# Optimization experiments

Measured on AMD Instinct MI355X. Metric: run time of the kernel, lower is better.

Reference implementation:

```python
import jax, jax.numpy as jnp
import numpy as np

B, D, V, T = 256, 1024, 32000, 64  # num_seqs, hidden dim, vocab, history len


def setup_inputs() -> dict:
    key = jax.random.key(0)
    ks = jax.random.split(key, 8)
    hidden = jax.random.normal(ks[0], (B, D), dtype=jnp.float32)
    embedding = jax.random.normal(ks[1], (V, D), dtype=jnp.float32) * (1.0 / np.sqrt(D))
    output_tokens = jax.random.randint(ks[2], (B, T), 0, V, dtype=jnp.int64)
    presence_penalties = jax.random.uniform(ks[3], (B,), dtype=jnp.float32)
    frequency_penalties = jax.random.uniform(ks[4], (B,), dtype=jnp.float32)
    temperatures = jax.random.uniform(ks[5], (B,), dtype=jnp.float32) + 0.5  # > eps
    top_ps = jax.random.uniform(ks[6], (B,), dtype=jnp.float32) * 0.5 + 0.5  # in [0.5, 1.0)
    top_ks = jax.random.randint(ks[7], (B,), 1, V, dtype=jnp.int64)
    return {
        "hidden": hidden,
        "embedding": embedding,
        "output_tokens": output_tokens,
        "presence_penalties": presence_penalties,
        "frequency_penalties": frequency_penalties,
        "temperatures": temperatures,
        "top_ps": top_ps,
        "top_ks": top_ks,
    }


def reference(hidden, embedding, output_tokens, presence_penalties,
              frequency_penalties, temperatures, top_ps, top_ks):
    # 1) logits = pruned hidden states @ embedding^T  -> [B, V]
    logits = jnp.einsum("bd,vd->bv", hidden, embedding)
    b, v = logits.shape

    # 2) presence/frequency penalties via per-row token histogram (np.bincount equiv)
    rows = jnp.broadcast_to(jnp.arange(b)[:, None], output_tokens.shape)
    counts = jnp.zeros((b, v), logits.dtype).at[rows, output_tokens].add(1.0)
    logits = logits - frequency_penalties[:, None] * counts \
                    - presence_penalties[:, None] * (counts > 0).astype(logits.dtype)

    # 3) temperature scaling
    logits = logits / temperatures[:, None]

    # 4) probabilities
    probs = jax.nn.softmax(logits, axis=-1)

    # 5) top-p / top-k: descending sort, cumsum masks, scatter back via inverse perm
    order = jnp.argsort(-probs, axis=-1)                       # descending order
    probs_sort = jnp.take_along_axis(probs, order, axis=-1)
    probs_cum = jnp.cumsum(probs_sort, axis=-1)
    top_p_mask = (probs_cum - probs_sort) > top_ps[:, None]
    top_k_mask = jnp.arange(v)[None, :] >= top_ks[:, None]
    probs_sort = jnp.where(top_p_mask | top_k_mask, 0.0, probs_sort)
    inv = jnp.argsort(order, axis=-1)
    filtered_probs = jnp.take_along_axis(probs_sort, inv, axis=-1)  # original order
    return filtered_probs
```

## Files before the change

### kernel.cpp

```cpp
#include <hip/hip_runtime.h>
#include <math.h>

#define NB 256
#define NV 32000
#define ND 1024
#define NT 64

#define GN 64
#define ASTR 56
#define NKB 64
#define ASLAB (256 * ASTR)
#define NGBLK (NV / GN)
#define INV2048F 4.8828125e-4f

#define NBIN 1024
#define FIX2 4294967296.0
#define PACK1 (1ull << 48)
#define SMASK ((1ull << 48) - 1ull)

typedef _Float16 f16x8 __attribute__((ext_vector_type(8)));
typedef _Float16 f16x4 __attribute__((ext_vector_type(4)));
typedef float f32x16 __attribute__((ext_vector_type(16)));
typedef __attribute__((address_space(3))) void lds_void;
typedef __attribute__((address_space(1))) void glb_void;

struct RowP2 {
  unsigned long long basePack;
  unsigned long long toppZfix;
  unsigned pfx;
  int ktop;
  float invZ;
  unsigned ustar;
  int m;
  int cEq;
};

__device__ __forceinline__ unsigned mono_enc(float f) {
  unsigned u = __float_as_uint(f);
  return (u & 0x80000000u) ? ~u : (u | 0x80000000u);
}
__device__ __forceinline__ float mono_dec(unsigned u) {
  return (u & 0x80000000u) ? __uint_as_float(u & 0x7FFFFFFFu) : __uint_as_float(~u);
}

__global__ __launch_bounds__(256) void convert_A(const float* __restrict__ hidden,
                                                 _Float16* __restrict__ A3) {
  const int kb = blockIdx.x, t = threadIdx.x;
  __shared__ _Float16 slab[ASLAB];
#pragma unroll
  for (int it = 0; it < 4; it++) {
    const int m = it * 64 + (t >> 2);
    const int k4 = (t & 3) * 4;
    float4 a4 = *(const float4*)(hidden + (size_t)m * ND + kb * 16 + k4);
    _Float16* base = slab + m * ASTR;
    float v[4] = {a4.x, a4.y, a4.z, a4.w};
#pragma unroll
    for (int q = 0; q < 4; q++) {
      const _Float16 h = (_Float16)v[q];
      const _Float16 l2 = (_Float16)((v[q] - (float)h) * 2048.0f);
      const int kk = k4 + q;
      base[kk] = h;
      base[16 + 2 * kk] = h;
      base[17 + 2 * kk] = l2;
    }
  }
  __syncthreads();
  const uint4* s = (const uint4*)slab;
  uint4* g = (uint4*)(A3 + (size_t)kb * ASLAB);
#pragma unroll
  for (int i = 0; i < 7; i++) g[i * 256 + t] = s[i * 256 + t];
}

__global__ __launch_bounds__(256, 2) void gemm_f16s(
    const float* __restrict__ Bm, const _Float16* __restrict__ A3,
    const float* __restrict__ temp, unsigned* __restrict__ rowmax,
    float* __restrict__ C) {
  __shared__ _Float16 Als[ASLAB];
  __shared__ _Float16 Bls[GN * ASTR];
  __shared__ float s_invT[256];
  __shared__ unsigned s_pm[256];

  const int t = threadIdx.x;
  const int l = t & 63, w = t >> 6;
  const int n0 = blockIdx.x * GN;
  s_invT[t] = 1.0f / temp[t];
  s_pm[t] = 0u;

  f32x16 accA[2][2] = {};
  f32x16 accB[2][2] = {};

  const int bn = t >> 2, bk4 = (t & 3) * 4;
  const int l31 = l & 31, lh = l >> 5;
  const int ka = lh * 8;
  const int mb = w * 64;

  for (int kb = 0; kb < NKB; kb++) {
    {
      const char* ga = (const char*)A3 + (size_t)kb * (ASLAB * 2) + (w * 7) * 1024 + l * 16;
      char* la = (char*)Als + (w * 7) * 1024;
#pragma unroll
      for (int i = 0; i < 7; i++)
        __builtin_amdgcn_global_load_lds((const glb_void*)(ga + i * 1024),
                                         (lds_void*)(la + i * 1024), 16, 0, 0);
    }
    {
      const float4 bv = *(const float4*)(Bm + (size_t)(n0 + bn) * ND + kb * 16 + bk4);
      const _Float16 h0 = (_Float16)bv.x, h1 = (_Float16)bv.y,
                     h2 = (_Float16)bv.z, h3 = (_Float16)bv.w;
      const _Float16 l0 = (_Float16)((bv.x - (float)h0) * 2048.0f);
      const _Float16 l1 = (_Float16)((bv.y - (float)h1) * 2048.0f);
      const _Float16 l2 = (_Float16)((bv.z - (float)h2) * 2048.0f);
      const _Float16 l3 = (_Float16)((bv.w - (float)h3) * 2048.0f);
      _Float16* prow = Bls + bn * ASTR;
      *(f16x4*)(prow + bk4) = (f16x4){h0, h1, h2, h3};
      *(f16x8*)(prow + 16 + 2 * bk4) = (f16x8){l0, h0, l1, h1, l2, h2, l3, h3};
    }
    __syncthreads();
    {
      const _Float16* Ap = Als + (size_t)(mb + l31) * ASTR + ka;
      const _Float16* Bp = Bls + (size_t)l31 * ASTR + ka;
      f16x8 a0 = *(const f16x8*)(Ap);
      f16x8 a1 = *(const f16x8*)(Ap + 32 * ASTR);
      f16x8 b0 = *(const f16x8*)(Bp);
      f16x8 b1 = *(const f16x8*)(Bp + 32 * ASTR);
      accA[0][0] = __builtin_amdgcn_mfma_f32_32x32x16_f16(a0, b0, accA[0][0], 0, 0, 0);
      accA[0][1] = __builtin_amdgcn_mfma_f32_32x32x16_f16(a0, b1, accA[0][1], 0, 0, 0);
      accA[1][0] = __builtin_amdgcn_mfma_f32_32x32x16_f16(a1, b0, accA[1][0], 0, 0, 0);
      accA[1][1] = __builtin_amdgcn_mfma_f32_32x32x16_f16(a1, b1, accA[1][1], 0, 0, 0);
#pragma unroll
      for (int s = 0; s < 2; s++) {
        const int off = 16 + s * 16;
        f16x8 c0 = *(const f16x8*)(Ap + off);
        f16x8 c1 = *(const f16x8*)(Ap + 32 * ASTR + off);
        f16x8 d0 = *(const f16x8*)(Bp + off);
        f16x8 d1 = *(const f16x8*)(Bp + 32 * ASTR + off);
        accB[0][0] = __builtin_amdgcn_mfma_f32_32x32x16_f16(c0, d0, accB[0][0], 0, 0, 0);
        accB[0][1] = __builtin_amdgcn_mfma_f32_32x32x16_f16(c0, d1, accB[0][1], 0, 0, 0);
        accB[1][0] = __builtin_amdgcn_mfma_f32_32x32x16_f16(c1, d0, accB[1][0], 0, 0, 0);
        accB[1][1] = __builtin_amdgcn_mfma_f32_32x32x16_f16(c1, d1, accB[1][1], 0, 0, 0);
      }
    }
    __syncthreads();
  }

#pragma unroll
  for (int mi = 0; mi < 2; mi++) {
#pragma unroll
    for (int r = 0; r < 16; r++) {
      const int row = mb + mi * 32 + (r & 3) + 8 * (r >> 2) + 4 * lh;
      const float it = s_invT[row];
      float v0 = (accA[mi][0][r] + accB[mi][0][r] * INV2048F) * it;
      float v1 = (accA[mi][1][r] + accB[mi][1][r] * INV2048F) * it;
      C[(size_t)row * NV + n0 + l31] = v0;
      C[(size_t)row * NV + n0 + 32 + l31] = v1;
      float mx = fmaxf(v0, v1);
#pragma unroll
      for (int o = 1; o < 32; o <<= 1) mx = fmaxf(mx, __shfl_xor(mx, o));
      if (l31 == 0) atomicMax(&s_pm[row], mono_enc(mx));
    }
  }
  __syncthreads();
  atomicMax(&rowmax[t], s_pm[t]);
}

__global__ __launch_bounds__(64) void s0_prep(
    const unsigned* __restrict__ rowmax, const int* __restrict__ toks,
    const float* __restrict__ pres, const float* __restrict__ freq,
    const float* __restrict__ temp, float* __restrict__ Mrow,
    float* __restrict__ buf) {
  const int b = blockIdx.x, t = threadIdx.x;
  __shared__ int s_tok[NT];
  s_tok[t] = toks[b * NT + t];
  __syncthreads();
  const int tk = s_tok[t];
  bool first = true; int cnt = 0;
  for (int j = 0; j < NT; j++)
    if (s_tok[j] == tk) { if (j < t) first = false; cnt++; }
  if (first)
    buf[(size_t)b * NV + tk] -= (freq[b] * (float)cnt + pres[b]) / temp[b];
  if (t == 0) Mrow[b] = mono_dec(rowmax[b]);
}

__global__ __launch_bounds__(256) void h_l0(
    float* __restrict__ buf, const float* __restrict__ Mrow,
    unsigned long long* __restrict__ histP) {
  const int b = blockIdx.x >> 3, sl = blockIdx.x & 7, t = threadIdx.x;
  __shared__ unsigned long long h[NBIN];
  for (int i = t; i < NBIN; i += 256) h[i] = 0ull;
  __syncthreads();
  const float M = Mrow[b];
  float* row = buf + (size_t)b * NV;
  const int base = sl * 4096;
#pragma unroll
  for (int it = 0; it < 4; it++) {
    const int idx = base + (it * 256 + t) * 4;
    if (idx < NV) {
      float4 x4 = *(const float4*)(row + idx);
      float4 e4;
      e4.x = expf(x4.x - M); e4.y = expf(x4.y - M);
      e4.z = expf(x4.z - M); e4.w = expf(x4.w - M);
      *(float4*)(row + idx) = e4;
      unsigned k;
      k = __float_as_uint(e4.x); if (k) atomicAdd(&h[k >> 20], PACK1 | (unsigned long long)(e4.x * FIX2));
      k = __float_as_uint(e4.y); if (k) atomicAdd(&h[k >> 20], PACK1 | (unsigned long long)(e4.y * FIX2));
      k = __float_as_uint(e4.z); if (k) atomicAdd(&h[k >> 20], PACK1 | (unsigned long long)(e4.z * FIX2));
      k = __float_as_uint(e4.w); if (k) atomicAdd(&h[k >> 20], PACK1 | (unsigned long long)(e4.w * FIX2));
    }
  }
  __syncthreads();
  unsigned long long* gh = histP + (size_t)b * NBIN;
  for (int i = t; i < NBIN; i += 256)
    if (h[i]) atomicAdd(&gh[i], h[i]);
}

__global__ __launch_bounds__(256) void h_ref(
    const float* __restrict__ buf, const RowP2* __restrict__ params,
    unsigned long long* __restrict__ histP, int matchShift, int binShift) {
  const int b = blockIdx.x >> 3, sl = blockIdx.x & 7, t = threadIdx.x;
  __shared__ unsigned long long h[NBIN];
  for (int i = t; i < NBIN; i += 256) h[i] = 0ull;
  __syncthreads();
  const unsigned pfx = params[b].pfx;
  const float* row = buf + (size_t)b * NV;
  const int base = sl * 4096;
#pragma unroll
  for (int it = 0; it < 4; it++) {
    const int idx = base + (it * 256 + t) * 4;
    if (idx < NV) {
      float4 e4 = *(const float4*)(row + idx);
      unsigned k;
      k = __float_as_uint(e4.x); if (k && (k >> matchShift) == pfx) atomicAdd(&h[(k >> binShift) & 1023u], PACK1 | (unsigned long long)(e4.x * FIX2));
      k = __float_as_uint(e4.y); if (k && (k >> matchShift) == pfx) atomicAdd(&h[(k >> binShift) & 1023u], PACK1 | (unsigned long long)(e4.y * FIX2));
      k = __float_as_uint(e4.z); if (k && (k >> matchShift) == pfx) atomicAdd(&h[(k >> binShift) & 1023u], PACK1 | (unsigned long long)(e4.z * FIX2));
      k = __float_as_uint(e4.w); if (k && (k >> matchShift) == pfx) atomicAdd(&h[(k >> binShift) & 1023u], PACK1 | (unsigned long long)(e4.w * FIX2));
    }
  }
  __syncthreads();
  unsigned long long* gh = histP + (size_t)b * NBIN;
  for (int i = t; i < NBIN; i += 256)
    if (h[i]) atomicAdd(&gh[i], h[i]);
}

__global__ __launch_bounds__(256) void s2_level(
    unsigned long long* __restrict__ histP, const float* __restrict__ topp_a,
    const int* __restrict__ topk_a, RowP2* __restrict__ params, int level) {
  const int b = blockIdx.x, t = threadIdx.x;
  __shared__ unsigned long long suf[NBIN];
  __shared__ unsigned long long sc[256];
  __shared__ int s_bs;
  unsigned long long* hp = histP + (size_t)b * NBIN;
  unsigned long long v[4];
#pragma unroll
  for (int i = 0; i < 4; i++) { v[i] = hp[t * 4 + i]; hp[t * 4 + i] = 0ull; }
  if (t == 0) s_bs = 1023;
  sc[t] = v[0] + v[1] + v[2] + v[3];
  __syncthreads();
  for (int off = 1; off < 256; off <<= 1) {
    unsigned long long add = (t + off < 256) ? sc[t + off] : 0ull;
    __syncthreads();
    sc[t] += add;
    __syncthreads();
  }
  const unsigned long long totalP = sc[0];
  unsigned long long run = (t < 255) ? sc[t + 1] : 0ull;
  suf[t * 4 + 3] = run; run += v[3];
  suf[t * 4 + 2] = run; run += v[2];
  suf[t * 4 + 1] = run; run += v[1];
  suf[t * 4 + 0] = run;
  __syncthreads();

  RowP2 p;
  unsigned long long base, toppZ;
  int ktop_;
  if (level == 0) {
    ktop_ = topk_a[b];
    unsigned long long Zfix = totalP & SMASK;
    if (!Zfix) Zfix = 1ull;
    toppZ = (unsigned long long)((double)topp_a[b] * (double)Zfix);
    base = 0ull;
    p.pfx = 0; p.invZ = (float)(FIX2 / (double)Zfix);
    p.ustar = 0; p.m = 0; p.cEq = 0;
  } else {
    p = params[b];
    base = p.basePack; toppZ = p.toppZfix; ktop_ = p.ktop;
  }

#pragma unroll
  for (int i = 0; i < 4; i++) {
    const int bin = t * 4 + i;
    const unsigned long long sG = base + suf[bin];
    const bool A = ((long long)(sG >> 48) < (long long)ktop_) && ((sG & SMASK) <= toppZ);
    const unsigned long long sPfull = base + ((bin > 0) ? suf[bin - 1] : totalP);
    const bool Ap = ((long long)(sPfull >> 48) < (long long)ktop_) && ((sPfull & SMASK) <= toppZ);
    if (A && !Ap) s_bs = bin;
  }
  __syncthreads();
  if (t == 0) {
    const int bs = s_bs;
    const unsigned long long newBase = base + suf[bs];
    if (level < 2) {
      p.basePack = newBase;
      p.toppZfix = toppZ;
      p.ktop = ktop_;
      p.pfx = (level == 0) ? (unsigned)bs : ((p.pfx << 10) | (unsigned)bs);
      params[b] = p;
    } else {
      const unsigned ustar = (p.pfx << 10) | (unsigned)bs;
      const unsigned long long raw = ((bs > 0) ? suf[bs - 1] : totalP) - suf[bs];
      const int cEq = (int)(raw >> 48);
      const long long Chi = (long long)(newBase >> 48);
      const unsigned long long Shi = newBase & SMASK;
      long long m = cEq;
      const long long lim = (long long)ktop_ - Chi;
      if (lim < m) m = lim;
      const double tf = (double)__uint_as_float(ustar) * FIX2;
      const double rem = (double)(toppZ - Shi);
      const double Rd = floor(rem / tf) + 1.0;
      if (Rd < (double)m) m = (long long)Rd;
      if (m < 1) m = 1;
      p.ustar = ustar; p.m = (int)m; p.cEq = cEq;
      params[b] = p;
    }
  }
}

__global__ __launch_bounds__(256) void s3_filter(
    float* __restrict__ buf, const RowP2* __restrict__ params) {
  const int b = blockIdx.x >> 3, sl = blockIdx.x & 7, t = threadIdx.x;
  const RowP2 p = params[b];
  const unsigned ustar = p.ustar;
  const float invZ = p.invZ;
  const bool need = (p.m < p.cEq);
  float* row = buf + (size_t)b * NV;
  const int base = sl * 4096;
#pragma unroll
  for (int it = 0; it < 4; it++) {
    const int idx = base + (it * 256 + t) * 4;
    if (idx < NV) {
      float4 e4 = *(const float4*)(row + idx);
      float4 o4;
      unsigned k;
      k = __float_as_uint(e4.x);
      o4.x = (k > ustar) ? e4.x * invZ : ((k == ustar) ? (need ? -e4.x : e4.x * invZ) : 0.f);
      k = __float_as_uint(e4.y);
      o4.y = (k > ustar) ? e4.y * invZ : ((k == ustar) ? (need ? -e4.y : e4.y * invZ) : 0.f);
      k = __float_as_uint(e4.z);
      o4.z = (k > ustar) ? e4.z * invZ : ((k == ustar) ? (need ? -e4.z : e4.z * invZ) : 0.f);
      k = __float_as_uint(e4.w);
      o4.w = (k > ustar) ? e4.w * invZ : ((k == ustar) ? (need ? -e4.w : e4.w * invZ) : 0.f);
      *(float4*)(row + idx) = o4;
    }
  }
}

__global__ __launch_bounds__(256) void s5_tie(
    float* __restrict__ buf, const RowP2* __restrict__ params) {
  const int b = blockIdx.x, t = threadIdx.x;
  const RowP2 p = params[b];
  if (p.m >= p.cEq) return;
  const int m = p.m;
  const float invZ = p.invZ;
  float* row = buf + (size_t)b * NV;
  __shared__ int s_rank[256];
  const int CH = NV / 256;
  const int base = t * CH, end = base + CH;
  int myc = 0;
  for (int v = base; v < end; v++) myc += (row[v] < 0.f);
  s_rank[t] = myc;
  __syncthreads();
  for (int off = 1; off < 256; off <<= 1) {
    const int v0 = s_rank[t];
    const int vn = (t >= off) ? s_rank[t - off] : 0;
    __syncthreads();
    s_rank[t] = v0 + vn;
    __syncthreads();
  }
  int r = (t > 0) ? s_rank[t - 1] : 0;
  for (int v = base; v < end; v++) {
    const float f = row[v];
    if (f < 0.f) {
      row[v] = (r < m) ? (-f) * invZ : 0.f;
      r++;
    }
  }
}

extern "C" void kernel_launch(void* const* d_in, const int* in_sizes, int n_in,
                              void* d_out, int out_size, void* d_ws, size_t ws_size,
                              hipStream_t stream) {
  (void)in_sizes; (void)n_in; (void)out_size; (void)ws_size;
  const float* hidden = (const float*)d_in[0];
  const float* emb    = (const float*)d_in[1];
  const int*   toks   = (const int*)d_in[2];
  const float* pres   = (const float*)d_in[3];
  const float* freq   = (const float*)d_in[4];
  const float* temp   = (const float*)d_in[5];
  const float* topp   = (const float*)d_in[6];
  const int*   topk   = (const int*)d_in[7];
  float* out = (float*)d_out;

  const size_t offA3   = 0;
  const size_t offRM   = 1835008;
  const size_t offHist = offRM + 1024;
  const size_t offMr   = offHist + 2097152;
  const size_t offPar  = offMr + 1024;

  _Float16* A3 = (_Float16*)((char*)d_ws + offA3);
  unsigned* rowmax = (unsigned*)((char*)d_ws + offRM);
  unsigned long long* histP = (unsigned long long*)((char*)d_ws + offHist);
  float* Mrow = (float*)((char*)d_ws + offMr);
  RowP2* params = (RowP2*)((char*)d_ws + offPar);

  hipMemsetAsync((char*)d_ws + offRM, 0, 1024 + 2097152, stream);
  convert_A<<<NKB, 256, 0, stream>>>(hidden, A3);
  gemm_f16s<<<NGBLK, 256, 0, stream>>>(emb, A3, temp, rowmax, out);
  s0_prep<<<NB, 64, 0, stream>>>(rowmax, toks, pres, freq, temp, Mrow, out);
  h_l0<<<NB * 8, 256, 0, stream>>>(out, Mrow, histP);
  s2_level<<<NB, 256, 0, stream>>>(histP, topp, topk, params, 0);
  h_ref<<<NB * 8, 256, 0, stream>>>(out, params, histP, 20, 10);
  s2_level<<<NB, 256, 0, stream>>>(histP, topp, topk, params, 1);
  h_ref<<<NB * 8, 256, 0, stream>>>(out, params, histP, 10, 0);
  s2_level<<<NB, 256, 0, stream>>>(histP, topp, topk, params, 2);
  s3_filter<<<NB * 8, 256, 0, stream>>>(out, params);
  s5_tie<<<NB, 256, 0, stream>>>(out, params);
}
```

Measured before the change: 333.3 us.

## Double-buffer GEMM LDS tiles with explicit waitcnt software pipelining

Splits the A and B LDS tiles into two buffers and restructures the K loop into a prefetching pipeline. The next A slab is loaded asynchronously into LDS and the next B row is prefetched into registers, both with manual vmcnt waits, while MFMA runs on the current buffer. This cuts the barriers per iteration from two to one and hides global load latency. It doubles LDS usage, which may lower occupancy at 2 blocks per CU. The hand-counted waitcnt values are fragile if the compiler reorders loads.

```diff
diff --git a/kernel.cpp b/kernel.cpp
--- a/kernel.cpp
+++ b/kernel.cpp
@@ -75,8 +75,8 @@
     const float* __restrict__ Bm, const _Float16* __restrict__ A3,
     const float* __restrict__ temp, unsigned* __restrict__ rowmax,
     float* __restrict__ C) {
-  __shared__ _Float16 Als[ASLAB];
-  __shared__ _Float16 Bls[GN * ASTR];
+  __shared__ _Float16 Als[2][ASLAB];
+  __shared__ _Float16 Bls[2][GN * ASTR];
   __shared__ float s_invT[256];
   __shared__ unsigned s_pm[256];
 
@@ -94,54 +94,109 @@
   const int ka = lh * 8;
   const int mb = w * 64;
 
-  for (int kb = 0; kb < NKB; kb++) {
-    {
-      const char* ga = (const char*)A3 + (size_t)kb * (ASLAB * 2) + (w * 7) * 1024 + l * 16;
-      char* la = (char*)Als + (w * 7) * 1024;
-#pragma unroll
-      for (int i = 0; i < 7; i++)
-        __builtin_amdgcn_global_load_lds((const glb_void*)(ga + i * 1024),
-                                         (lds_void*)(la + i * 1024), 16, 0, 0);
-    }
-    {
-      const float4 bv = *(const float4*)(Bm + (size_t)(n0 + bn) * ND + kb * 16 + bk4);
-      const _Float16 h0 = (_Float16)bv.x, h1 = (_Float16)bv.y,
-                     h2 = (_Float16)bv.z, h3 = (_Float16)bv.w;
-      const _Float16 l0 = (_Float16)((bv.x - (float)h0) * 2048.0f);
-      const _Float16 l1 = (_Float16)((bv.y - (float)h1) * 2048.0f);
-      const _Float16 l2 = (_Float16)((bv.z - (float)h2) * 2048.0f);
-      const _Float16 l3 = (_Float16)((bv.w - (float)h3) * 2048.0f);
-      _Float16* prow = Bls + bn * ASTR;
-      *(f16x4*)(prow + bk4) = (f16x4){h0, h1, h2, h3};
-      *(f16x8*)(prow + 16 + 2 * bk4) = (f16x8){l0, h0, l1, h1, l2, h2, l3, h3};
-    }
-    __syncthreads();
-    {
-      const _Float16* Ap = Als + (size_t)(mb + l31) * ASTR + ka;
-      const _Float16* Bp = Bls + (size_t)l31 * ASTR + ka;
-      f16x8 a0 = *(const f16x8*)(Ap);
-      f16x8 a1 = *(const f16x8*)(Ap + 32 * ASTR);
-      f16x8 b0 = *(const f16x8*)(Bp);
-      f16x8 b1 = *(const f16x8*)(Bp + 32 * ASTR);
-      accA[0][0] = __builtin_amdgcn_mfma_f32_32x32x16_f16(a0, b0, accA[0][0], 0, 0, 0);
-      accA[0][1] = __builtin_amdgcn_mfma_f32_32x32x16_f16(a0, b1, accA[0][1], 0, 0, 0);
-      accA[1][0] = __builtin_amdgcn_mfma_f32_32x32x16_f16(a1, b0, accA[1][0], 0, 0, 0);
-      accA[1][1] = __builtin_amdgcn_mfma_f32_32x32x16_f16(a1, b1, accA[1][1], 0, 0, 0);
-#pragma unroll
-      for (int s = 0; s < 2; s++) {
-        const int off = 16 + s * 16;
-        f16x8 c0 = *(const f16x8*)(Ap + off);
-        f16x8 c1 = *(const f16x8*)(Ap + 32 * ASTR + off);
-        f16x8 d0 = *(const f16x8*)(Bp + off);
-        f16x8 d1 = *(const f16x8*)(Bp + 32 * ASTR + off);
-        accB[0][0] = __builtin_amdgcn_mfma_f32_32x32x16_f16(c0, d0, accB[0][0], 0, 0, 0);
-        accB[0][1] = __builtin_amdgcn_mfma_f32_32x32x16_f16(c0, d1, accB[0][1], 0, 0, 0);
-        accB[1][0] = __builtin_amdgcn_mfma_f32_32x32x16_f16(c1, d0, accB[1][0], 0, 0, 0);
-        accB[1][1] = __builtin_amdgcn_mfma_f32_32x32x16_f16(c1, d1, accB[1][1], 0, 0, 0);
-      }
-    }
-    __syncthreads();
-  }
+  const float* browp = Bm + (size_t)(n0 + bn) * ND + bk4;
+  const char* gaBase = (const char*)A3 + (w * 7) * 1024 + l * 16;
+  char* laB0 = (char*)&Als[0][0] + (w * 7) * 1024;
+  char* laB1 = (char*)&Als[1][0] + (w * 7) * 1024;
+
+#define ISSUE_A(kbn, LA)                                                        \
+  do {                                                                          \
+    const char* ga_ = gaBase + (size_t)(kbn) * (ASLAB * 2);                     \
+    _Pragma("unroll") for (int i_ = 0; i_ < 7; i_++)                            \
+        __builtin_amdgcn_global_load_lds((const glb_void*)(ga_ + i_ * 1024),    \
+                                         (lds_void*)((LA) + i_ * 1024), 16, 0,  \
+                                         0);                                    \
+  } while (0)
+
+#define BCONV(BV, DST)                                                          \
+  do {                                                                          \
+    const _Float16 h0_ = (_Float16)(BV).x, h1_ = (_Float16)(BV).y,              \
+                   h2_ = (_Float16)(BV).z, h3_ = (_Float16)(BV).w;              \
+    const _Float16 q0_ = (_Float16)(((BV).x - (float)h0_) * 2048.0f);           \
+    const _Float16 q1_ = (_Float16)(((BV).y - (float)h1_) * 2048.0f);           \
+    const _Float16 q2_ = (_Float16)(((BV).z - (float)h2_) * 2048.0f);           \
+    const _Float16 q3_ = (_Float16)(((BV).w - (float)h3_) * 2048.0f);           \
+    _Float16* prow_ = (DST) + bn * ASTR;                                        \
+    *(f16x4*)(prow_ + bk4) = (f16x4){h0_, h1_, h2_, h3_};                       \
+    *(f16x8*)(prow_ + 16 + 2 * bk4) =                                           \
+        (f16x8){q0_, h0_, q1_, h1_, q2_, h2_, q3_, h3_};                        \
+  } while (0)
+
+#define COMPUTE(CUR)                                                                       \
+  do {                                                                                     \
+    const _Float16* Ap_ = &Als[CUR][0] + (size_t)(mb + l31) * ASTR + ka;                   \
+    const _Float16* Bp_ = &Bls[CUR][0] + (size_t)l31 * ASTR + ka;                          \
+    f16x8 a0_ = *(const f16x8*)(Ap_);                                                      \
+    f16x8 a1_ = *(const f16x8*)(Ap_ + 32 * ASTR);                                          \
+    f16x8 b0_ = *(const f16x8*)(Bp_);                                                      \
+    f16x8 b1_ = *(const f16x8*)(Bp_ + 32 * ASTR);                                          \
+    accA[0][0] = __builtin_amdgcn_mfma_f32_32x32x16_f16(a0_, b0_, accA[0][0], 0, 0, 0);    \
+    accA[0][1] = __builtin_amdgcn_mfma_f32_32x32x16_f16(a0_, b1_, accA[0][1], 0, 0, 0);    \
+    accA[1][0] = __builtin_amdgcn_mfma_f32_32x32x16_f16(a1_, b0_, accA[1][0], 0, 0, 0);    \
+    accA[1][1] = __builtin_amdgcn_mfma_f32_32x32x16_f16(a1_, b1_, accA[1][1], 0, 0, 0);    \
+    _Pragma("unroll") for (int s_ = 0; s_ < 2; s_++) {                                     \
+      const int off_ = 16 + s_ * 16;                                                       \
+      f16x8 c0_ = *(const f16x8*)(Ap_ + off_);                                             \
+      f16x8 c1_ = *(const f16x8*)(Ap_ + 32 * ASTR + off_);                                 \
+      f16x8 d0_ = *(const f16x8*)(Bp_ + off_);                                             \
+      f16x8 d1_ = *(const f16x8*)(Bp_ + 32 * ASTR + off_);                                 \
+      accB[0][0] = __builtin_amdgcn_mfma_f32_32x32x16_f16(c0_, d0_, accB[0][0], 0, 0, 0);  \
+      accB[0][1] = __builtin_amdgcn_mfma_f32_32x32x16_f16(c0_, d1_, accB[0][1], 0, 0, 0);  \
+      accB[1][0] = __builtin_amdgcn_mfma_f32_32x32x16_f16(c1_, d0_, accB[1][0], 0, 0, 0);  \
+      accB[1][1] = __builtin_amdgcn_mfma_f32_32x32x16_f16(c1_, d1_, accB[1][1], 0, 0, 0);  \
+    }                                                                                      \
+  } while (0)
+
+  ISSUE_A(0, laB0);
+  __builtin_amdgcn_sched_barrier(0);
+  float4 bv0 = *(const float4*)(browp);
+  __builtin_amdgcn_sched_barrier(0);
+  float4 bvA = *(const float4*)(browp + 16);
+  __builtin_amdgcn_sched_barrier(0);
+  asm volatile("s_waitcnt vmcnt(1)" ::: "memory");
+  BCONV(bv0, &Bls[0][0]);
+  asm volatile("s_waitcnt lgkmcnt(0)\ns_barrier" ::: "memory");
+
+  float4 bvB;
+  for (int kb = 0; kb < 62; kb += 2) {
+    ISSUE_A(kb + 1, laB1);
+    __builtin_amdgcn_sched_barrier(0);
+    bvB = *(const float4*)(browp + (size_t)(kb + 2) * 16);
+    __builtin_amdgcn_sched_barrier(0);
+    asm volatile("s_waitcnt vmcnt(9)" ::: "memory");
+    COMPUTE(0);
+    __builtin_amdgcn_sched_barrier(0);
+    asm volatile("s_waitcnt vmcnt(8)" ::: "memory");
+    BCONV(bvA, &Bls[1][0]);
+    asm volatile("s_waitcnt lgkmcnt(0)\ns_barrier" ::: "memory");
+
+    ISSUE_A(kb + 2, laB0);
+    __builtin_amdgcn_sched_barrier(0);
+    bvA = *(const float4*)(browp + (size_t)(kb + 3) * 16);
+    __builtin_amdgcn_sched_barrier(0);
+    asm volatile("s_waitcnt vmcnt(9)" ::: "memory");
+    COMPUTE(1);
+    __builtin_amdgcn_sched_barrier(0);
+    asm volatile("s_waitcnt vmcnt(8)" ::: "memory");
+    BCONV(bvB, &Bls[0][0]);
+    asm volatile("s_waitcnt lgkmcnt(0)\ns_barrier" ::: "memory");
+  }
+
+  ISSUE_A(63, laB1);
+  __builtin_amdgcn_sched_barrier(0);
+  asm volatile("s_waitcnt vmcnt(8)" ::: "memory");
+  COMPUTE(0);
+  __builtin_amdgcn_sched_barrier(0);
+  asm volatile("s_waitcnt vmcnt(7)" ::: "memory");
+  BCONV(bvA, &Bls[1][0]);
+  asm volatile("s_waitcnt lgkmcnt(0)\ns_barrier" ::: "memory");
+
+  asm volatile("s_waitcnt vmcnt(0)" ::: "memory");
+  COMPUTE(1);
+
+#undef ISSUE_A
+#undef BCONV
+#undef COMPUTE
 
 #pragma unroll
   for (int mi = 0; mi < 2; mi++) {
```

Result: faster. 319.5 us (-4.2%).
